# Optimization experiments

Hardware: AMD Instinct MI355X
Metric: run time of the kernel (lower is better)

## Reference

```python
import jax, jax.numpy as jnp
import numpy as np

B, L, D = 2048, 200, 128
N_ITEMS = 100000


def _lin(k, fan_in, fan_out):
    s = 1.0 / np.sqrt(fan_in)
    kw, kb = jax.random.split(k)
    w = jax.random.uniform(kw, (fan_in, fan_out), jnp.float32, -s, s)
    b = jax.random.uniform(kb, (fan_out,), jnp.float32, -s, s)
    return w, b


def setup_inputs() -> dict:
    key = jax.random.key(0)
    ks = jax.random.split(key, 12)
    item_emb = jax.random.normal(ks[0], (N_ITEMS, D), jnp.float32).at[0].set(0.0)  # padding_idx=0
    item_bias_tab = jax.random.normal(ks[1], (N_ITEMS, 1), jnp.float32).at[0].set(0.0)
    aw1, ab1 = _lin(ks[2], 3 * D, 128)
    aw2, ab2 = _lin(ks[3], 128, 64)
    afw, afb = _lin(ks[4], 64, 1)
    nw, nb = _lin(ks[5], D, D)
    dw1, db1 = _lin(ks[6], 3 * D, 512)
    dw2, db2 = _lin(ks[7], 512, 256)
    dw3, db3 = _lin(ks[8], 256, 128)
    fw, fb = _lin(ks[9], 128, 1)
    in_item_id = jax.random.randint(ks[10], (B, L), 0, N_ITEMS, dtype=jnp.int32)
    item_id = jax.random.randint(ks[11], (B,), 0, N_ITEMS, dtype=jnp.int32)
    return dict(in_item_id=in_item_id, item_id=item_id, item_emb=item_emb,
                item_bias_tab=item_bias_tab, aw1=aw1, ab1=ab1, aw2=aw2, ab2=ab2,
                afw=afw, afb=afb, nw=nw, nb=nb, dw1=dw1, db1=db1, dw2=dw2, db2=db2,
                dw3=dw3, db3=db3, fw=fw, fb=fb)


def reference(in_item_id, item_id, item_emb, item_bias_tab,
              aw1, ab1, aw2, ab2, afw, afb, nw, nb,
              dw1, db1, dw2, db2, dw3, db3, fw, fb):
    sig = jax.nn.sigmoid
    seq_emb = item_emb[in_item_id]          # [B, L, D]
    target_emb = item_emb[item_id]          # [B, D]
    item_bias = item_bias_tab[item_id][:, 0]  # [B]

    t = target_emb[:, None, :]              # [B, 1, D] broadcast over L
    key = jnp.concatenate((jnp.broadcast_to(t, seq_emb.shape),
                           t * seq_emb,
                           t - seq_emb), axis=-1)  # [B, L, 3D]

    # feed-forward (DIN) attention scorer: MLP(key) -> scalar score per position
    h = sig(key @ aw1 + ab1)
    h = sig(h @ aw2 + ab2)
    score = (h @ afw + afb)[..., 0]         # [B, L]
    score = jnp.where(in_item_id == 0, 0.0, score)  # key_padding_mask, softmax=False
    attn_seq = jnp.einsum('bl,bld->bd', score, seq_emb)  # [B, D]

    attn_seq = attn_seq @ nw + nb           # norm Linear
    cat_emb = jnp.concatenate((attn_seq, target_emb, target_emb * attn_seq), axis=-1)  # [B, 3D]
    g = sig(cat_emb @ dw1 + db1)
    g = sig(g @ dw2 + db2)
    g = sig(g @ dw3 + db3)
    out = (g @ fw + fb)[:, 0]               # [B]
    return out + item_bias
```

## Files before the change

### kernel.cpp

```cpp
#include <hip/hip_runtime.h>
#include <hip/hip_bf16.h>
#include <stdint.h>

typedef __attribute__((ext_vector_type(8))) short bf8;
typedef __attribute__((ext_vector_type(4))) short bf4;
typedef __attribute__((ext_vector_type(4))) float f32x4;

#define MFMA16(a,b,c) __builtin_amdgcn_mfma_f32_16x16x32_bf16(a,b,c,0,0,0)

__device__ __forceinline__ unsigned short f2bf(float x){
  unsigned int u = __builtin_bit_cast(unsigned int, x);
  u = u + 0x7FFFu + ((u >> 16) & 1u);
  return (unsigned short)(u >> 16);
}
__device__ __forceinline__ unsigned short f2bfb(float x){
  __hip_bfloat16 h = __float2bfloat16(x);
  return __builtin_bit_cast(unsigned short, h);
}
__device__ __forceinline__ float bf2f(unsigned short h){
  unsigned int u = ((unsigned int)h) << 16;
  return __builtin_bit_cast(float, u);
}
__device__ __forceinline__ float sigm(float x){
  return __builtin_amdgcn_rcpf(1.0f + __expf(-x));
}
__device__ __forceinline__ int swzu(int row, int k, int Kd8){
  return (row*Kd8 + ((k>>3) ^ (row & 7)))*8 + (k & 7);
}

__device__ __forceinline__ void tile_transpose(const float* __restrict__ in,
                                               unsigned short* __restrict__ out,
                                               int R, int C, int tb,
                                               float* tile, int tid)
{
  int nkt = R >> 6;
  int kt = tb % nkt, jt = tb / nkt;
  int r0 = tid >> 4, cs = tid & 15;
  #pragma unroll
  for (int i = 0; i < 4; ++i){
    int r = r0 + i*16;
    float4 v = *(const float4*)(in + (size_t)(kt*64 + r)*C + jt*64 + cs*4);
    tile[r*65 + cs*4 + 0] = v.x;
    tile[r*65 + cs*4 + 1] = v.y;
    tile[r*65 + cs*4 + 2] = v.z;
    tile[r*65 + cs*4 + 3] = v.w;
  }
  __syncthreads();
  int j = tid >> 2, ks = tid & 3;
  bf8 o0, o1;
  #pragma unroll
  for (int e = 0; e < 8; ++e){
    o0[e] = (short)f2bf(tile[(ks*16 + e)*65 + j]);
    o1[e] = (short)f2bf(tile[(ks*16 + 8 + e)*65 + j]);
  }
  *(bf8*)(out + (size_t)(jt*64 + j)*R + kt*64 + ks*16)     = o0;
  *(bf8*)(out + (size_t)(jt*64 + j)*R + kt*64 + ks*16 + 8) = o1;
}

__global__ void k_prep(const float* __restrict__ aw1, const float* __restrict__ aw2,
                       const float* __restrict__ nw, const float* __restrict__ dw1,
                       const float* __restrict__ dw2, const float* __restrict__ dw3,
                       const float* __restrict__ emb,
                       unsigned short* __restrict__ WbT, unsigned short* __restrict__ WcT,
                       unsigned short* __restrict__ Wsum, unsigned short* __restrict__ A2T,
                       unsigned short* __restrict__ NWT, unsigned short* __restrict__ D1T,
                       unsigned short* __restrict__ D2T, unsigned short* __restrict__ D3T,
                       unsigned short* __restrict__ EMBB)
{
  __shared__ float tile[64*65];
  const int bid = blockIdx.x;
  const int tid = threadIdx.x;

  if (bid < 88){
    if (bid < 48)      tile_transpose(dw1, D1T, 384, 512, bid,      tile, tid);
    else if (bid < 80) tile_transpose(dw2, D2T, 512, 256, bid - 48, tile, tid);
    else               tile_transpose(dw3, D3T, 256, 128, bid - 80, tile, tid);
    return;
  }

  int n = (bid - 88)*256 + tid;
  int stride = (gridDim.x - 88)*256;
  for (int i = n; i < 1600000; i += stride){
    const float4* s = (const float4*)(emb + (size_t)i*8);
    float4 a = s[0], b = s[1];
    bf8 o;
    o[0]=(short)f2bf(a.x); o[1]=(short)f2bf(a.y); o[2]=(short)f2bf(a.z); o[3]=(short)f2bf(a.w);
    o[4]=(short)f2bf(b.x); o[5]=(short)f2bf(b.y); o[6]=(short)f2bf(b.z); o[7]=(short)f2bf(b.w);
    ((bf8*)EMBB)[i] = o;
  }
  for (int i = n; i < 16384; i += stride){
    int j = i >> 7, k = i & 127;
    WbT[i] = f2bf(aw1[(128+k)*128 + j]);
    WcT[i] = f2bf(aw1[(256+k)*128 + j]);
  }
  for (int i = n; i < 16384; i += stride){
    int j = i >> 7, k = i & 127;
    Wsum[i] = f2bf(aw1[k*128 + j] + aw1[(256+k)*128 + j]);
  }
  for (int i = n; i < 8192; i += stride){
    int j = i >> 7, k = i & 127;
    A2T[i] = f2bf(aw2[k*64 + j]);
  }
  for (int i = n; i < 16384; i += stride){
    int j = i >> 7, k = i & 127;
    NWT[i] = f2bf(nw[k*128 + j]);
  }
}

__global__ __launch_bounds__(256) void k_attn(
    const int* __restrict__ in_ids, const int* __restrict__ item_id,
    const float* __restrict__ emb, const unsigned short* __restrict__ embb,
    const float* __restrict__ ab1, const float* __restrict__ ab2v,
    const float* __restrict__ afw, const float* __restrict__ afb,
    const unsigned short* __restrict__ WbT, const unsigned short* __restrict__ WcT,
    const unsigned short* __restrict__ Wsum, const unsigned short* __restrict__ A2T,
    float* __restrict__ attn_raw)
{
  __shared__ __align__(16) unsigned short sS[32*128];
  __shared__ __align__(16) unsigned short sH[32*128];
  __shared__ float sT[128];
  __shared__ float sC0[128];
  __shared__ float sP2[2][128];
  __shared__ float sPart[4][32];
  __shared__ int   sIds[32];

  const int b = blockIdx.x;
  const int tid = threadIdx.x;
  const int wave = tid >> 6, lane = tid & 63;
  const int lr = lane & 15, lg = lane >> 4;

  const int tgt = item_id[b];
  if (tid < 128) sT[tid] = emb[(size_t)tgt*128 + tid];
  __syncthreads();

  {
    int j = tid & 127, hf = tid >> 7;
    const unsigned short* wsrow = Wsum + j*128 + hf*64;
    float p = 0.f;
    #pragma unroll
    for (int c = 0; c < 8; ++c){
      bf8 wv = *(const bf8*)(wsrow + c*8);
      #pragma unroll
      for (int e = 0; e < 8; ++e)
        p += sT[hf*64 + c*8 + e] * bf2f((unsigned short)wv[e]);
    }
    sP2[hf][j] = p;
  }
  __syncthreads();
  if (tid < 128) sC0[tid] = ab1[tid] + sP2[0][tid] + sP2[1][tid];

  bf8 wfrag[2][4];
  {
    const float4* sT4 = (const float4*)sT;
    #pragma unroll
    for (int mt = 0; mt < 2; ++mt){
      int j = (wave + mt*4)*16 + lr;
      #pragma unroll
      for (int kk = 0; kk < 4; ++kk){
        bf8 wb = *(const bf8*)(WbT + j*128 + kk*32 + lg*8);
        bf8 wc = *(const bf8*)(WcT + j*128 + kk*32 + lg*8);
        float4 t0 = sT4[kk*8 + lg*2];
        float4 t1 = sT4[kk*8 + lg*2 + 1];
        float tv[8] = {t0.x,t0.y,t0.z,t0.w,t1.x,t1.y,t1.z,t1.w};
        bf8 o;
        #pragma unroll
        for (int e = 0; e < 8; ++e)
          o[e] = (short)f2bfb(tv[e]*bf2f((unsigned short)wb[e]) - bf2f((unsigned short)wc[e]));
        wfrag[mt][kk] = o;
      }
    }
  }
  bf8 a2frag[4];
  #pragma unroll
  for (int kk = 0; kk < 4; ++kk)
    a2frag[kk] = *(const bf8*)(A2T + (wave*16+lr)*128 + kk*32 + lg*8);

  float b2r[4], afr[4];
  #pragma unroll
  for (int i = 0; i < 4; ++i){
    int j2 = wave*16 + lg*4 + i;
    b2r[i] = ab2v[j2];
    afr[i] = afw[j2];
  }
  const float afbv = afb[0];
  __syncthreads();
  float c0r[2][4];
  #pragma unroll
  for (int mt = 0; mt < 2; ++mt)
    #pragma unroll
    for (int i = 0; i < 4; ++i)
      c0r[mt][i] = sC0[(wave + mt*4)*16 + lg*4 + i];

  float facc8[8] = {0,0,0,0,0,0,0,0};
  const bf8* S8 = (const bf8*)sS;
  const bf8* H8 = (const bf8*)sH;
  const int rg = tid >> 4, cg = tid & 15;
  const int sxm = lr & 7;
  const int chv = tid & 15;
  const int rowq = tid >> 4;

  bf8 stg0, stg1; int id0, id1;
  {
    id0 = in_ids[b*200 + rowq];
    stg0 = *(const bf8*)(embb + (size_t)id0*128 + chv*8);
    id1 = in_ids[b*200 + 16 + rowq];
    stg1 = *(const bf8*)(embb + (size_t)id1*128 + chv*8);
  }

  for (int rt = 0; rt < 7; ++rt){
    __syncthreads();
    if (chv == 0){ sIds[rowq] = id0; sIds[16 + rowq] = id1; }
    ((bf8*)sS)[rowq*16 + (chv ^ (rowq & 7))] = stg0;
    {
      int r2 = 16 + rowq;
      ((bf8*)sS)[r2*16 + (chv ^ (r2 & 7))] = stg1;
    }
    if (rt < 6){
      int l0 = (rt+1)*32 + rowq;
      id0 = (l0 < 200) ? in_ids[b*200 + l0] : 0;
      stg0 = *(const bf8*)(embb + (size_t)id0*128 + chv*8);
      int l1 = l0 + 16;
      id1 = (l1 < 200) ? in_ids[b*200 + l1] : 0;
      stg1 = *(const bf8*)(embb + (size_t)id1*128 + chv*8);
    }
    __syncthreads();
    f32x4 acc1[2][2] = {};
    #pragma unroll
    for (int kk = 0; kk < 4; ++kk){
      int kx = (kk*4 + lg) ^ sxm;
      bf8 s0 = S8[lr*16 + kx];
      bf8 s1 = S8[(16+lr)*16 + kx];
      acc1[0][0] = MFMA16(wfrag[0][kk], s0, acc1[0][0]);
      acc1[0][1] = MFMA16(wfrag[0][kk], s1, acc1[0][1]);
      acc1[1][0] = MFMA16(wfrag[1][kk], s0, acc1[1][0]);
      acc1[1][1] = MFMA16(wfrag[1][kk], s1, acc1[1][1]);
    }
    #pragma unroll
    for (int mt = 0; mt < 2; ++mt)
      #pragma unroll
      for (int nt = 0; nt < 2; ++nt){
        int r = nt*16 + lr;
        int j0 = (wave + mt*4)*16 + lg*4;
        bf4 q4;
        #pragma unroll
        for (int i = 0; i < 4; ++i)
          q4[i] = (short)f2bfb(sigm(acc1[mt][nt][i] + c0r[mt][i]));
        int idx = (r*16 + ((j0 >> 3) ^ (r & 7)))*8 + (j0 & 7);
        *(bf4*)(sH + idx) = q4;
      }
    __syncthreads();
    f32x4 acc2[2] = {};
    #pragma unroll
    for (int kk = 0; kk < 4; ++kk){
      int kx = (kk*4 + lg) ^ sxm;
      bf8 h0 = H8[lr*16 + kx];
      bf8 h1f = H8[(16+lr)*16 + kx];
      acc2[0] = MFMA16(a2frag[kk], h0, acc2[0]);
      acc2[1] = MFMA16(a2frag[kk], h1f, acc2[1]);
    }
    float part0 = 0.f, part1 = 0.f;
    #pragma unroll
    for (int i = 0; i < 4; ++i){
      part0 += sigm(acc2[0][i] + b2r[i]) * afr[i];
      part1 += sigm(acc2[1][i] + b2r[i]) * afr[i];
    }
    part0 += __shfl_xor(part0, 16); part0 += __shfl_xor(part0, 32);
    part1 += __shfl_xor(part1, 16); part1 += __shfl_xor(part1, 32);
    if (lg == 0){ sPart[wave][lr] = part0; sPart[wave][16+lr] = part1; }
    __syncthreads();
    #pragma unroll
    for (int q = 0; q < 2; ++q){
      int r = rg*2 + q;
      int l = rt*32 + r;
      float sc = sPart[0][r] + sPart[1][r] + sPart[2][r] + sPart[3][r] + afbv;
      sc = (l < 200 && sIds[r] != 0) ? sc : 0.f;
      bf8 v = S8[r*16 + (cg ^ (r & 7))];
      #pragma unroll
      for (int e = 0; e < 8; ++e)
        facc8[e] += sc * bf2f((unsigned short)v[e]);
    }
  }
  __syncthreads();
  float* red = (float*)sS;
  #pragma unroll
  for (int e = 0; e < 8; ++e) red[tid*8 + e] = facc8[e];
  __syncthreads();
  if (tid < 128){
    float s = 0.f;
    #pragma unroll
    for (int g = 0; g < 16; ++g) s += red[g*128 + tid];
    attn_raw[(size_t)b*128 + tid] = s;
  }
}

__global__ __launch_bounds__(512) void k_deep(
    const int* __restrict__ item_id, const float* __restrict__ emb,
    const float* __restrict__ bias_tab,
    const float* __restrict__ nbv,
    const float* __restrict__ db1, const float* __restrict__ db2,
    const float* __restrict__ db3, const float* __restrict__ fw,
    const float* __restrict__ fb,
    const unsigned short* __restrict__ NWT, const unsigned short* __restrict__ D1T,
    const unsigned short* __restrict__ D2T, const unsigned short* __restrict__ D3T,
    const float* __restrict__ attn_raw, float* __restrict__ out)
{
  __shared__ __align__(16) unsigned short sA[16*128];
  __shared__ float sTf[16*128];
  __shared__ __align__(16) unsigned short sCat[16*384];
  __shared__ __align__(16) unsigned short sG1[16*512];
  __shared__ __align__(16) unsigned short sG2[16*256];
  __shared__ __align__(16) unsigned short sG3[16*128];
  __shared__ float sNB[128], sDB1[512], sDB2[256], sDB3[128], sFWd[128];
  __shared__ float sBias[16];

  const int r0 = blockIdx.x * 16;
  const int tid = threadIdx.x;
  const int wave = tid >> 6, lane = tid & 63;
  const int lr = lane & 15, lg = lane >> 4;
  const int sx = lr & 7;

  if (tid < 128){ sNB[tid] = nbv[tid]; sDB3[tid] = db3[tid]; sFWd[tid] = fw[tid]; }
  sDB1[tid] = db1[tid];
  if (tid < 256) sDB2[tid] = db2[tid];
  if (tid < 16) sBias[tid] = bias_tab[item_id[r0 + tid]];

  if (tid < 256){
    int r = tid >> 4, ch = tid & 15;
    const float* asrc = attn_raw + (size_t)(r0 + r)*128 + ch*8;
    float4 v0 = *(const float4*)asrc;
    float4 v1 = *(const float4*)(asrc + 4);
    bf8 o;
    o[0]=(short)f2bf(v0.x); o[1]=(short)f2bf(v0.y); o[2]=(short)f2bf(v0.z); o[3]=(short)f2bf(v0.w);
    o[4]=(short)f2bf(v1.x); o[5]=(short)f2bf(v1.y); o[6]=(short)f2bf(v1.z); o[7]=(short)f2bf(v1.w);
    ((bf8*)sA)[r*16 + (ch ^ (r & 7))] = o;
    int id = item_id[r0 + r];
    const float* tsrc = emb + (size_t)id*128 + ch*8;
    float4 t0 = *(const float4*)tsrc;
    float4 t1 = *(const float4*)(tsrc + 4);
    *(float4*)(sTf + r*128 + ch*8)     = t0;
    *(float4*)(sTf + r*128 + ch*8 + 4) = t1;
  }
  __syncthreads();

  {
    const bf8* A8 = (const bf8*)sA;
    int ct = wave;
    f32x4 acc = {};
    #pragma unroll
    for (int kk = 0; kk < 4; ++kk){
      int kx = (kk*4 + lg) ^ sx;
      bf8 af = A8[lr*16 + kx];
      bf8 bw = *(const bf8*)(NWT + (ct*16+lr)*128 + kk*32 + lg*8);
      acc = MFMA16(af, bw, acc);
    }
    int col = ct*16 + lr;
    float nbc = sNB[col];
    #pragma unroll
    for (int i = 0; i < 4; ++i){
      int r = lg*4 + i;
      float x = acc[i] + nbc;
      float tv = sTf[r*128 + col];
      sCat[swzu(r, col,      48)] = f2bf(x);
      sCat[swzu(r, 128+col,  48)] = f2bf(tv);
      sCat[swzu(r, 256+col,  48)] = f2bf(tv * x);
    }
  }
  __syncthreads();
  {
    const bf8* C8 = (const bf8*)sCat;
    #pragma unroll
    for (int c = 0; c < 4; ++c){
      int ct = wave + c*8;
      f32x4 acc = {};
      #pragma unroll
      for (int kk = 0; kk < 12; ++kk){
        int kx = (kk*4 + lg) ^ sx;
        bf8 af = C8[lr*48 + kx];
        bf8 bw = *(const bf8*)(D1T + (size_t)(ct*16+lr)*384 + kk*32 + lg*8);
        acc = MFMA16(af, bw, acc);
      }
      int col = ct*16 + lr;
      float bb = sDB1[col];
      #pragma unroll
      for (int i = 0; i < 4; ++i)
        sG1[swzu(lg*4 + i, col, 64)] = f2bf(sigm(acc[i] + bb));
    }
  }
  __syncthreads();
  {
    const bf8* G8 = (const bf8*)sG1;
    #pragma unroll
    for (int c = 0; c < 2; ++c){
      int ct = wave + c*8;
      f32x4 acc = {};
      #pragma unroll
      for (int kk = 0; kk < 16; ++kk){
        int kx = (kk*4 + lg) ^ sx;
        bf8 af = G8[lr*64 + kx];
        bf8 bw = *(const bf8*)(D2T + (size_t)(ct*16+lr)*512 + kk*32 + lg*8);
        acc = MFMA16(af, bw, acc);
      }
      int col = ct*16 + lr;
      float bb = sDB2[col];
      #pragma unroll
      for (int i = 0; i < 4; ++i)
        sG2[swzu(lg*4 + i, col, 32)] = f2bf(sigm(acc[i] + bb));
    }
  }
  __syncthreads();
  {
    const bf8* G8 = (const bf8*)sG2;
    int ct = wave;
    f32x4 acc = {};
    #pragma unroll
    for (int kk = 0; kk < 8; ++kk){
      int kx = (kk*4 + lg) ^ sx;
      bf8 af = G8[lr*32 + kx];
      bf8 bw = *(const bf8*)(D3T + (size_t)(ct*16+lr)*256 + kk*32 + lg*8);
      acc = MFMA16(af, bw, acc);
    }
    int col = ct*16 + lr;
    float bb = sDB3[col];
    #pragma unroll
    for (int i = 0; i < 4; ++i)
      sG3[swzu(lg*4 + i, col, 16)] = f2bf(sigm(acc[i] + bb));
  }
  __syncthreads();
  if (tid < 128){
    int r = tid >> 3, seg = tid & 7;
    float p = 0.f;
    #pragma unroll
    for (int c = 0; c < 16; ++c)
      p += bf2f(sG3[swzu(r, seg*16 + c, 16)]) * sFWd[seg*16 + c];
    p += __shfl_xor(p, 1);
    p += __shfl_xor(p, 2);
    p += __shfl_xor(p, 4);
    if (seg == 0) out[r0 + r] = p + fb[0] + sBias[r];
  }
}

extern "C" void kernel_launch(void* const* d_in, const int* in_sizes, int n_in,
                              void* d_out, int out_size, void* d_ws, size_t ws_size,
                              hipStream_t stream) {
  const int*   in_ids   = (const int*)d_in[0];
  const int*   item_id  = (const int*)d_in[1];
  const float* emb      = (const float*)d_in[2];
  const float* bias_tab = (const float*)d_in[3];
  const float* aw1 = (const float*)d_in[4];
  const float* ab1 = (const float*)d_in[5];
  const float* aw2 = (const float*)d_in[6];
  const float* ab2 = (const float*)d_in[7];
  const float* afw = (const float*)d_in[8];
  const float* afb = (const float*)d_in[9];
  const float* nw  = (const float*)d_in[10];
  const float* nb  = (const float*)d_in[11];
  const float* dw1 = (const float*)d_in[12];
  const float* db1 = (const float*)d_in[13];
  const float* dw2 = (const float*)d_in[14];
  const float* db2 = (const float*)d_in[15];
  const float* dw3 = (const float*)d_in[16];
  const float* db3 = (const float*)d_in[17];
  const float* fw  = (const float*)d_in[18];
  const float* fb  = (const float*)d_in[19];
  float* outp = (float*)d_out;

  char* ws = (char*)d_ws;
  float* attn_raw = (float*)ws;
  unsigned short* WbT  = (unsigned short*)(ws + 1048576);
  unsigned short* WcT  = WbT  + 16384;
  unsigned short* Wsum = WcT  + 16384;
  unsigned short* A2T  = Wsum + 16384;
  unsigned short* NWT  = A2T  + 8192;
  unsigned short* D1T  = NWT  + 16384;
  unsigned short* D2T  = D1T  + 196608;
  unsigned short* D3T  = D2T  + 131072;
  unsigned short* EMBB = D3T  + 32768;

  hipLaunchKernelGGL(k_prep, dim3(2048), dim3(256), 0, stream,
                     aw1, aw2, nw, dw1, dw2, dw3, emb,
                     WbT, WcT, Wsum, A2T, NWT, D1T, D2T, D3T, EMBB);
  hipLaunchKernelGGL(k_attn, dim3(2048), dim3(256), 0, stream,
                     in_ids, item_id, emb, EMBB, ab1, ab2, afw, afb,
                     WbT, WcT, Wsum, A2T, attn_raw);
  hipLaunchKernelGGL(k_deep, dim3(128), dim3(512), 0, stream,
                     item_id, emb, bias_tab, nb, db1, db2, db3, fw, fb,
                     NWT, D1T, D2T, D3T, attn_raw, outp);
}
```

Measured before the change: 111.5 us.

## Use 512 threads in attention kernel, splitting MFMA work across eight waves

The attention scorer kernel now runs 8 waves per block instead of 4. Each wave computes one 16-column tile of the first MLP layer and one row-half of the second layer, and each thread stages and accumulates a single embedding row chunk. The goal is more latency hiding and fewer registers per thread (one weight fragment set instead of two). The cost is a larger final reduction over 32 partials and more block-level synchronisation among more waves.

Measured after the change: 117.7 us. 1.06x slower.

```diff
diff --git a/kernel.cpp b/kernel.cpp
--- a/kernel.cpp
+++ b/kernel.cpp
@@ -107,7 +107,7 @@
   }
 }
 
-__global__ __launch_bounds__(256) void k_attn(
+__global__ __launch_bounds__(512) void k_attn(
     const int* __restrict__ in_ids, const int* __restrict__ item_id,
     const float* __restrict__ emb, const unsigned short* __restrict__ embb,
     const float* __restrict__ ab1, const float* __restrict__ ab2v,
@@ -116,24 +116,28 @@
     const unsigned short* __restrict__ Wsum, const unsigned short* __restrict__ A2T,
     float* __restrict__ attn_raw)
 {
-  __shared__ __align__(16) unsigned short sS[32*128];
-  __shared__ __align__(16) unsigned short sH[32*128];
+  __shared__ __align__(16) unsigned short sSH[2][32*128];
   __shared__ float sT[128];
   __shared__ float sC0[128];
   __shared__ float sP2[2][128];
   __shared__ float sPart[4][32];
   __shared__ int   sIds[32];
 
+  unsigned short* sS = sSH[0];
+  unsigned short* sH = sSH[1];
+
   const int b = blockIdx.x;
   const int tid = threadIdx.x;
   const int wave = tid >> 6, lane = tid & 63;
   const int lr = lane & 15, lg = lane >> 4;
+  const int wh = wave & 3;
+  const int rh = wave >> 2;
 
   const int tgt = item_id[b];
   if (tid < 128) sT[tid] = emb[(size_t)tgt*128 + tid];
   __syncthreads();
 
-  {
+  if (tid < 256){
     int j = tid & 127, hf = tid >> 7;
     const unsigned short* wsrow = Wsum + j*128 + hf*64;
     float p = 0.f;
@@ -149,146 +153,121 @@
   __syncthreads();
   if (tid < 128) sC0[tid] = ab1[tid] + sP2[0][tid] + sP2[1][tid];
 
-  bf8 wfrag[2][4];
+  bf8 wfrag[4];
   {
     const float4* sT4 = (const float4*)sT;
-    #pragma unroll
-    for (int mt = 0; mt < 2; ++mt){
-      int j = (wave + mt*4)*16 + lr;
-      #pragma unroll
-      for (int kk = 0; kk < 4; ++kk){
-        bf8 wb = *(const bf8*)(WbT + j*128 + kk*32 + lg*8);
-        bf8 wc = *(const bf8*)(WcT + j*128 + kk*32 + lg*8);
-        float4 t0 = sT4[kk*8 + lg*2];
-        float4 t1 = sT4[kk*8 + lg*2 + 1];
-        float tv[8] = {t0.x,t0.y,t0.z,t0.w,t1.x,t1.y,t1.z,t1.w};
-        bf8 o;
-        #pragma unroll
-        for (int e = 0; e < 8; ++e)
-          o[e] = (short)f2bfb(tv[e]*bf2f((unsigned short)wb[e]) - bf2f((unsigned short)wc[e]));
-        wfrag[mt][kk] = o;
-      }
+    int j = wave*16 + lr;
+    #pragma unroll
+    for (int kk = 0; kk < 4; ++kk){
+      bf8 wb = *(const bf8*)(WbT + j*128 + kk*32 + lg*8);
+      bf8 wc = *(const bf8*)(WcT + j*128 + kk*32 + lg*8);
+      float4 t0 = sT4[kk*8 + lg*2];
+      float4 t1 = sT4[kk*8 + lg*2 + 1];
+      float tv[8] = {t0.x,t0.y,t0.z,t0.w,t1.x,t1.y,t1.z,t1.w};
+      bf8 o;
+      #pragma unroll
+      for (int e = 0; e < 8; ++e)
+        o[e] = (short)f2bfb(tv[e]*bf2f((unsigned short)wb[e]) - bf2f((unsigned short)wc[e]));
+      wfrag[kk] = o;
     }
   }
   bf8 a2frag[4];
   #pragma unroll
   for (int kk = 0; kk < 4; ++kk)
-    a2frag[kk] = *(const bf8*)(A2T + (wave*16+lr)*128 + kk*32 + lg*8);
+    a2frag[kk] = *(const bf8*)(A2T + (wh*16+lr)*128 + kk*32 + lg*8);
 
   float b2r[4], afr[4];
   #pragma unroll
   for (int i = 0; i < 4; ++i){
-    int j2 = wave*16 + lg*4 + i;
+    int j2 = wh*16 + lg*4 + i;
     b2r[i] = ab2v[j2];
     afr[i] = afw[j2];
   }
   const float afbv = afb[0];
   __syncthreads();
-  float c0r[2][4];
-  #pragma unroll
-  for (int mt = 0; mt < 2; ++mt)
-    #pragma unroll
-    for (int i = 0; i < 4; ++i)
-      c0r[mt][i] = sC0[(wave + mt*4)*16 + lg*4 + i];
+  float c0r[4];
+  #pragma unroll
+  for (int i = 0; i < 4; ++i)
+    c0r[i] = sC0[wave*16 + lg*4 + i];
 
   float facc8[8] = {0,0,0,0,0,0,0,0};
   const bf8* S8 = (const bf8*)sS;
   const bf8* H8 = (const bf8*)sH;
-  const int rg = tid >> 4, cg = tid & 15;
   const int sxm = lr & 7;
   const int chv = tid & 15;
   const int rowq = tid >> 4;
 
-  bf8 stg0, stg1; int id0, id1;
+  bf8 stg0; int id0;
   {
     id0 = in_ids[b*200 + rowq];
     stg0 = *(const bf8*)(embb + (size_t)id0*128 + chv*8);
-    id1 = in_ids[b*200 + 16 + rowq];
-    stg1 = *(const bf8*)(embb + (size_t)id1*128 + chv*8);
   }
 
   for (int rt = 0; rt < 7; ++rt){
     __syncthreads();
-    if (chv == 0){ sIds[rowq] = id0; sIds[16 + rowq] = id1; }
+    if (chv == 0) sIds[rowq] = id0;
     ((bf8*)sS)[rowq*16 + (chv ^ (rowq & 7))] = stg0;
-    {
-      int r2 = 16 + rowq;
-      ((bf8*)sS)[r2*16 + (chv ^ (r2 & 7))] = stg1;
-    }
     if (rt < 6){
       int l0 = (rt+1)*32 + rowq;
       id0 = (l0 < 200) ? in_ids[b*200 + l0] : 0;
       stg0 = *(const bf8*)(embb + (size_t)id0*128 + chv*8);
-      int l1 = l0 + 16;
-      id1 = (l1 < 200) ? in_ids[b*200 + l1] : 0;
-      stg1 = *(const bf8*)(embb + (size_t)id1*128 + chv*8);
     }
     __syncthreads();
-    f32x4 acc1[2][2] = {};
+    f32x4 acc1[2] = {};
     #pragma unroll
     for (int kk = 0; kk < 4; ++kk){
       int kx = (kk*4 + lg) ^ sxm;
       bf8 s0 = S8[lr*16 + kx];
       bf8 s1 = S8[(16+lr)*16 + kx];
-      acc1[0][0] = MFMA16(wfrag[0][kk], s0, acc1[0][0]);
-      acc1[0][1] = MFMA16(wfrag[0][kk], s1, acc1[0][1]);
-      acc1[1][0] = MFMA16(wfrag[1][kk], s0, acc1[1][0]);
-      acc1[1][1] = MFMA16(wfrag[1][kk], s1, acc1[1][1]);
-    }
-    #pragma unroll
-    for (int mt = 0; mt < 2; ++mt)
-      #pragma unroll
-      for (int nt = 0; nt < 2; ++nt){
-        int r = nt*16 + lr;
-        int j0 = (wave + mt*4)*16 + lg*4;
-        bf4 q4;
-        #pragma unroll
-        for (int i = 0; i < 4; ++i)
-          q4[i] = (short)f2bfb(sigm(acc1[mt][nt][i] + c0r[mt][i]));
-        int idx = (r*16 + ((j0 >> 3) ^ (r & 7)))*8 + (j0 & 7);
-        *(bf4*)(sH + idx) = q4;
-      }
+      acc1[0] = MFMA16(wfrag[kk], s0, acc1[0]);
+      acc1[1] = MFMA16(wfrag[kk], s1, acc1[1]);
+    }
+    #pragma unroll
+    for (int nt = 0; nt < 2; ++nt){
+      int r = nt*16 + lr;
+      int j0 = wave*16 + lg*4;
+      bf4 q4;
+      #pragma unroll
+      for (int i = 0; i < 4; ++i)
+        q4[i] = (short)f2bfb(sigm(acc1[nt][i] + c0r[i]));
+      int idx = (r*16 + ((j0 >> 3) ^ (r & 7)))*8 + (j0 & 7);
+      *(bf4*)(sH + idx) = q4;
+    }
     __syncthreads();
-    f32x4 acc2[2] = {};
+    f32x4 acc2 = {};
     #pragma unroll
     for (int kk = 0; kk < 4; ++kk){
       int kx = (kk*4 + lg) ^ sxm;
-      bf8 h0 = H8[lr*16 + kx];
-      bf8 h1f = H8[(16+lr)*16 + kx];
-      acc2[0] = MFMA16(a2frag[kk], h0, acc2[0]);
-      acc2[1] = MFMA16(a2frag[kk], h1f, acc2[1]);
-    }
-    float part0 = 0.f, part1 = 0.f;
-    #pragma unroll
-    for (int i = 0; i < 4; ++i){
-      part0 += sigm(acc2[0][i] + b2r[i]) * afr[i];
-      part1 += sigm(acc2[1][i] + b2r[i]) * afr[i];
-    }
-    part0 += __shfl_xor(part0, 16); part0 += __shfl_xor(part0, 32);
-    part1 += __shfl_xor(part1, 16); part1 += __shfl_xor(part1, 32);
-    if (lg == 0){ sPart[wave][lr] = part0; sPart[wave][16+lr] = part1; }
+      bf8 hf = H8[(rh*16 + lr)*16 + kx];
+      acc2 = MFMA16(a2frag[kk], hf, acc2);
+    }
+    float part = 0.f;
+    #pragma unroll
+    for (int i = 0; i < 4; ++i)
+      part += sigm(acc2[i] + b2r[i]) * afr[i];
+    part += __shfl_xor(part, 16); part += __shfl_xor(part, 32);
+    if (lg == 0) sPart[wh][rh*16 + lr] = part;
     __syncthreads();
-    #pragma unroll
-    for (int q = 0; q < 2; ++q){
-      int r = rg*2 + q;
+    {
+      int r = rowq;
       int l = rt*32 + r;
       float sc = sPart[0][r] + sPart[1][r] + sPart[2][r] + sPart[3][r] + afbv;
       sc = (l < 200 && sIds[r] != 0) ? sc : 0.f;
-      bf8 v = S8[r*16 + (cg ^ (r & 7))];
+      bf8 v = S8[r*16 + (chv ^ (r & 7))];
       #pragma unroll
       for (int e = 0; e < 8; ++e)
         facc8[e] += sc * bf2f((unsigned short)v[e]);
     }
   }
   __syncthreads();
-  float* red = (float*)sS;
+  float* red = (float*)sSH;
   #pragma unroll
   for (int e = 0; e < 8; ++e) red[tid*8 + e] = facc8[e];
   __syncthreads();
   if (tid < 128){
     float s = 0.f;
     #pragma unroll
-    for (int g = 0; g < 16; ++g) s += red[g*128 + tid];
+    for (int g = 0; g < 32; ++g) s += red[g*128 + tid];
     attn_raw[(size_t)b*128 + tid] = s;
   }
 }
@@ -479,7 +458,7 @@
   hipLaunchKernelGGL(k_prep, dim3(2048), dim3(256), 0, stream,
                      aw1, aw2, nw, dw1, dw2, dw3, emb,
                      WbT, WcT, Wsum, A2T, NWT, D1T, D2T, D3T, EMBB);
-  hipLaunchKernelGGL(k_attn, dim3(2048), dim3(256), 0, stream,
+  hipLaunchKernelGGL(k_attn, dim3(2048), dim3(512), 0, stream,
                      in_ids, item_id, emb, EMBB, ab1, ab2, afw, afb,
                      WbT, WcT, Wsum, A2T, attn_raw);
   hipLaunchKernelGGL(k_deep, dim3(128), dim3(512), 0, stream,
```
